# Kernel optimization log

Hardware: AMD Instinct MI355X
Metric: run time of the kernel (lower is better)

The kernel has to match this reference:

```python
import jax, jax.numpy as jnp
import numpy as np


def setup_inputs() -> dict:
    key = jax.random.key(0)
    k1, k2, k3 = jax.random.split(key, 3)
    B, L, D = 8, 4096, 320
    CB_DIM, N_BOOKS = 16, 8192
    input_values = jax.random.normal(k1, (B, L, D), dtype=jnp.float32)
    # mask all ones -> static masked-select shape N = B*L
    mask_time_indices = jnp.ones((B, L), dtype=jnp.int32)
    # xavier_uniform for Linear(D -> CB_DIM, bias=False): limit = sqrt(6/(fan_in+fan_out))
    limit = float(np.sqrt(6.0 / (D + CB_DIM)))
    proj_weight = jax.random.uniform(k2, (CB_DIM, D), dtype=jnp.float32, minval=-limit, maxval=limit)
    code_book = jax.random.normal(k3, (N_BOOKS, CB_DIM), dtype=jnp.float32)
    return {"input_values": input_values, "mask_time_indices": mask_time_indices,
            "proj_weight": proj_weight, "code_book": code_book}


def reference(input_values, mask_time_indices, proj_weight, code_book):
    # input_values: [B, L, D]; mask is all-ones so masked select == flatten (static shape N=B*L)
    B, L, D = input_values.shape
    flat = input_values.reshape(B * L, D)  # [N, D]
    targets = flat @ proj_weight.T  # [N, cb_dim]  (random projection, no bias)
    # argmin over Euclidean norm == argmin over squared distance (monotone),
    # expanded form avoids the [N, n_books, cb_dim] broadcast intermediate.
    t2 = jnp.sum(targets * targets, axis=-1, keepdims=True)        # [N, 1]
    c2 = jnp.sum(code_book * code_book, axis=-1)                   # [n_books]
    d2 = t2 - 2.0 * (targets @ code_book.T) + c2                   # [N, n_books]
    labels = jnp.argmin(d2, axis=-1)                               # [N]
    return labels
```

## Files before the change

### kernel.cpp

```cpp
#include <hip/hip_runtime.h>

#define N_ROWS 32768
#define D_IN 320
#define CB 16
#define N_BOOKS 8192

typedef __attribute__((ext_vector_type(8))) short bf16x8;
typedef __attribute__((ext_vector_type(4))) float f32x4;
#define MFMA __builtin_amdgcn_mfma_f32_16x16x32_bf16
#define AS1 __attribute__((address_space(1)))
#define AS3 __attribute__((address_space(3)))

__device__ __forceinline__ unsigned short bf16rn(float f) {
  unsigned u = __float_as_uint(f);
  u += 0x7fffu + ((u >> 16) & 1u);
  return (unsigned short)(u >> 16);
}
__device__ __forceinline__ float bf16tof(unsigned short h) {
  return __uint_as_float(((unsigned)h) << 16);
}
__device__ __forceinline__ void gload_lds16(const short* g, short* l) {
  __builtin_amdgcn_global_load_lds((const AS1 unsigned int*)g, (AS3 unsigned int*)l, 16, 0, 0);
}

__global__ __launch_bounds__(256, 2) void proj_prep_kernel(
    const float* __restrict__ x, const float* __restrict__ w, short* __restrict__ tsplit,
    const float* __restrict__ cbk, short* __restrict__ bfrag, float* __restrict__ nh_g,
    int* __restrict__ ctr) {
  __shared__ __align__(16) short wfrag[3][10][64][8];
  __shared__ __align__(16) float xs[2][64 * 36];
  const int tid = threadIdx.x;

  if (blockIdx.x >= 512) {
    const int bid = blockIdx.x - 512;
    if (bid == 0 && tid == 0) *ctr = 0;
    const int j = bid * 256 + tid;
    const float4* src = (const float4*)(cbk + (size_t)j * CB);
    float4 a = src[0], b = src[1], c = src[2], d = src[3];
    float ce[16] = {a.x, a.y, a.z, a.w, b.x, b.y, b.z, b.w,
                    c.x, c.y, c.z, c.w, d.x, d.y, d.z, d.w};
    short c1[16], c2[16];
    double s = 0.0;
#pragma unroll
    for (int i = 0; i < 16; i++) {
      s += (double)ce[i] * (double)ce[i];
      unsigned short x1 = bf16rn(ce[i]);
      float r1 = ce[i] - bf16tof(x1);
      unsigned short x2 = bf16rn(r1);
      c1[i] = (short)x1; c2[i] = (short)x2;
    }
    nh_g[j] = (float)(-0.5 * s);
    bf16x8 lo1, hi1, lo2, hi2;
#pragma unroll
    for (int i = 0; i < 8; i++) {
      lo1[i] = c1[i]; hi1[i] = c1[i + 8];
      lo2[i] = c2[i]; hi2[i] = c2[i + 8];
    }
    const int bt = j >> 4, n = j & 15;
    short* base = bfrag + (size_t)bt * 1024;
    *(bf16x8*)(base + (0 * 16 + n) * 8) = lo1;
    *(bf16x8*)(base + (1 * 16 + n) * 8) = hi1;
    *(bf16x8*)(base + (2 * 16 + n) * 8) = lo1;
    *(bf16x8*)(base + (3 * 16 + n) * 8) = hi1;
    *(bf16x8*)(base + 512 + (0 * 16 + n) * 8) = lo2;
    *(bf16x8*)(base + 512 + (1 * 16 + n) * 8) = hi2;
    *(bf16x8*)(base + 512 + (2 * 16 + n) * 8) = lo2;
    *(bf16x8*)(base + 512 + (3 * 16 + n) * 8) = hi2;
    return;
  }

  const int lane = tid & 63;
  const int wv = tid >> 6;

  for (int i = tid; i < D_IN * CB; i += 256) {
    int d = i >> 4, o = i & 15;
    float f = w[o * D_IN + d];
    unsigned short h1 = bf16rn(f);
    float r1 = f - bf16tof(h1);
    unsigned short h2 = bf16rn(r1);
    float r2 = r1 - bf16tof(h2);
    unsigned short h3 = bf16rn(r2);
    int c = d >> 5, qq = (d >> 3) & 3, pos = d & 7;
    int ln = qq * 16 + o;
    wfrag[0][c][ln][pos] = (short)h1;
    wfrag[1][c][ln][pos] = (short)h2;
    wfrag[2][c][ln][pos] = (short)h3;
  }

  const float* xblk = x + (size_t)blockIdx.x * 64 * D_IN;
  {
    int row = tid >> 2, k0 = (tid & 3) * 8;
    float4 v0 = *(const float4*)(xblk + row * D_IN + k0);
    float4 v1 = *(const float4*)(xblk + row * D_IN + k0 + 4);
    *(float4*)&xs[0][row * 36 + k0] = v0;
    *(float4*)&xs[0][row * 36 + k0 + 4] = v1;
  }
  __syncthreads();

  const int m = lane & 15, q = lane >> 4;
  f32x4 g1 = {0.f, 0.f, 0.f, 0.f}, g2 = {0.f, 0.f, 0.f, 0.f}, g3 = {0.f, 0.f, 0.f, 0.f};
  for (int c = 0; c < 10; c++) {
    const int buf = c & 1;
    if (c < 9) {
      int row = tid >> 2, k0 = (tid & 3) * 8;
      float4 v0 = *(const float4*)(xblk + row * D_IN + (c + 1) * 32 + k0);
      float4 v1 = *(const float4*)(xblk + row * D_IN + (c + 1) * 32 + k0 + 4);
      *(float4*)&xs[buf ^ 1][row * 36 + k0] = v0;
      *(float4*)&xs[buf ^ 1][row * 36 + k0 + 4] = v1;
    }
    const float* xp = &xs[buf][(wv * 16 + m) * 36 + q * 8];
    float4 xa = *(const float4*)xp;
    float4 xb = *(const float4*)(xp + 4);
    float xe[8] = {xa.x, xa.y, xa.z, xa.w, xb.x, xb.y, xb.z, xb.w};
    bf16x8 a1, a2, a3;
#pragma unroll
    for (int j = 0; j < 8; j++) {
      unsigned short h1 = bf16rn(xe[j]);
      float r1 = xe[j] - bf16tof(h1);
      unsigned short h2 = bf16rn(r1);
      float r2 = r1 - bf16tof(h2);
      unsigned short h3 = bf16rn(r2);
      a1[j] = (short)h1; a2[j] = (short)h2; a3[j] = (short)h3;
    }
    bf16x8 b1 = *(const bf16x8*)wfrag[0][c][lane];
    bf16x8 b2 = *(const bf16x8*)wfrag[1][c][lane];
    bf16x8 b3 = *(const bf16x8*)wfrag[2][c][lane];
    g1 = MFMA(a1, b1, g1, 0, 0, 0);
    g2 = MFMA(a2, b1, g2, 0, 0, 0);
    g2 = MFMA(a1, b2, g2, 0, 0, 0);
    g3 = MFMA(a3, b1, g3, 0, 0, 0);
    g3 = MFMA(a1, b3, g3, 0, 0, 0);
    g3 = MFMA(a2, b2, g3, 0, 0, 0);
    __syncthreads();
  }

  float* tl = (float*)xs;
#pragma unroll
  for (int r = 0; r < 4; r++) {
    double t = (double)g1[r] + ((double)g2[r] + (double)g3[r]);
    tl[(wv * 16 + q * 4 + r) * 17 + m] = (float)t;
  }
  __syncthreads();
  {
    int row_l = tid >> 2, p = tid & 3;
    short h1[4], h2[4], h3[4];
#pragma unroll
    for (int i = 0; i < 4; i++) {
      float f = tl[row_l * 17 + p * 4 + i];
      unsigned short a = bf16rn(f);
      float r1 = f - bf16tof(a);
      unsigned short b = bf16rn(r1);
      float r2 = r1 - bf16tof(b);
      unsigned short cc = bf16rn(r2);
      h1[i] = (short)a; h2[i] = (short)b; h3[i] = (short)cc;
    }
    size_t base = (size_t)(blockIdx.x * 64 + row_l) * 48;
    *(short4*)(tsplit + base + p * 4) = make_short4(h1[0], h1[1], h1[2], h1[3]);
    *(short4*)(tsplit + base + 16 + p * 4) = make_short4(h2[0], h2[1], h2[2], h2[3]);
    *(short4*)(tsplit + base + 32 + p * 4) = make_short4(h3[0], h3[1], h3[2], h3[3]);
  }
}

#define SC_H 16

__global__ __launch_bounds__(256, 4) void score_kernel(const short* __restrict__ tsplit,
                                                       const short* __restrict__ bfrag,
                                                       const float* __restrict__ nh_g,
                                                       float4* __restrict__ cand) {
  __shared__ __align__(16) short ldsb[2][4096];
  __shared__ float ldsnh[512];
  const int tid = threadIdx.x;
  const int lane = tid & 63;
  const int wv = tid >> 6;
  const int m = lane & 15, q = lane >> 4;
  const int rb = blockIdx.x & 127;
  const int h = blockIdx.x >> 7;
  const int rowbase = rb * 256;

  bf16x8 A12[4];
#pragma unroll
  for (int rt = 0; rt < 4; rt++) {
    int row = rowbase + wv * 64 + rt * 16 + m;
    A12[rt] = *(const bf16x8*)(tsplit + (size_t)row * 48 + q * 8);
  }
  for (int i = tid; i < 512; i += 256) ldsnh[i] = nh_g[h * 512 + i];

  const short* gq = bfrag + (size_t)h * 32768;
  {
    const short* g0 = gq + wv * 512 + lane * 8;
#pragma unroll
    for (int it = 0; it < 2; it++)
      gload_lds16(g0 + it * 2048, &ldsb[0][it * 2048 + wv * 512]);
  }

  float s1[4][4], s2[4][4];
  int i1[4][4];
#pragma unroll
  for (int rt = 0; rt < 4; rt++)
#pragma unroll
    for (int r = 0; r < 4; r++) { s1[rt][r] = -3.4e38f; s2[rt][r] = -3.4e38f; i1[rt][r] = 0; }

  __syncthreads();

  for (int sc = 0; sc < 8; sc++) {
    const int cur = sc & 1;
    if (sc < 7) {
      const short* gs = gq + (sc + 1) * 4096 + wv * 512 + lane * 8;
#pragma unroll
      for (int it = 0; it < 2; it++)
        gload_lds16(gs + it * 2048, &ldsb[cur ^ 1][it * 2048 + wv * 512]);
    }
#pragma unroll
    for (int bt = 0; bt < 4; bt++) {
      const short* bp = &ldsb[cur][bt * 1024];
      bf16x8 b1 = *(const bf16x8*)(bp + lane * 8);
      bf16x8 b2 = *(const bf16x8*)(bp + 512 + lane * 8);
      const int btg = sc * 4 + bt;
      float nh0 = ldsnh[btg * 16 + m];
      f32x4 ci = {nh0, nh0, nh0, nh0};
      const int colv = h * 512 + btg * 16 + m;
#pragma unroll
      for (int rt = 0; rt < 4; rt++) {
        f32x4 acc = MFMA(A12[rt], b1, ci, 0, 0, 0);
        acc = MFMA(A12[rt], b2, acc, 0, 0, 0);
#pragma unroll
        for (int r = 0; r < 4; r++) {
          float v = acc[r];
          float s1o = s1[rt][r];
          s2[rt][r] = __builtin_amdgcn_fmed3f(v, s1o, s2[rt][r]);
          s1[rt][r] = fmaxf(s1o, v);
          i1[rt][r] = (v > s1o) ? colv : i1[rt][r];
        }
      }
    }
    __syncthreads();
  }

#pragma unroll
  for (int rt = 0; rt < 4; rt++)
#pragma unroll
    for (int r = 0; r < 4; r++) {
      float a1v = s1[rt][r], a2v = s2[rt][r];
      int ai = i1[rt][r];
#pragma unroll
      for (int msk = 1; msk <= 8; msk <<= 1) {
        float o1 = __shfl_xor(a1v, msk);
        float o2 = __shfl_xor(a2v, msk);
        int oi = __shfl_xor(ai, msk);
        if (o1 > a1v) {
          a2v = fmaxf(a1v, o2); a1v = o1; ai = oi;
        } else {
          a2v = fmaxf(a2v, o1);
          if (o1 == a1v && oi < ai) ai = oi;
        }
      }
      if (m == 0) {
        int row = rowbase + wv * 64 + rt * 16 + q * 4 + r;
        cand[(size_t)h * N_ROWS + row] = make_float4(a1v, a2v, __int_as_float(ai), 0.f);
      }
    }
}

#define MARGIN_EPS 1.0e-3f

__global__ __launch_bounds__(256) void merge_flag_kernel(const float4* __restrict__ cand,
                                                         int* __restrict__ out,
                                                         int* __restrict__ list,
                                                         int* __restrict__ ctr) {
  const int r = blockIdx.x * 256 + threadIdx.x;
  float S1 = -3.4e38f, S2 = -3.4e38f;
  int I = 0;
#pragma unroll
  for (int h = 0; h < SC_H; h++) {
    float4 v = cand[(size_t)h * N_ROWS + r];
    if (v.x > S1) {
      S2 = fmaxf(S1, v.y); S1 = v.x; I = __float_as_int(v.z);
    } else {
      S2 = fmaxf(S2, v.x);
    }
  }
  out[r] = I;
  if (S1 - S2 < MARGIN_EPS) {
    int slot = atomicAdd(ctr, 1);
    list[slot] = r;
  }
}

__global__ __launch_bounds__(256) void rescore_kernel(const int* __restrict__ list,
                                                      const int* __restrict__ ctr,
                                                      const float* __restrict__ x,
                                                      const float* __restrict__ w,
                                                      const float* __restrict__ codebook,
                                                      int* __restrict__ out) {
  __shared__ double ps[16][17];
  __shared__ double tsh[16];
  __shared__ double rs[256];
  __shared__ int ri[256];
  const int tid = threadIdx.x;
  const int total = ctr[0];

  for (int it = blockIdx.x; it < total; it += gridDim.x) {
    const int row = list[it];
    {
      int o = tid & 15, c = tid >> 4;
      double p = 0.0;
      for (int k = 0; k < 20; k++) {
        int d = c * 20 + k;
        p = fma((double)x[(size_t)row * D_IN + d], (double)w[o * D_IN + d], p);
      }
      ps[c][o] = p;
    }
    __syncthreads();
    if (tid < 16) {
      double t = 0.0;
      for (int c = 0; c < 16; c++) t += ps[c][tid];
      tsh[tid] = t;
    }
    __syncthreads();
    double t[16];
#pragma unroll
    for (int i = 0; i < 16; i++) t[i] = tsh[i];
    double bs = -1.0e300;
    int bi = 0;
    for (int j = tid; j < N_BOOKS; j += 256) {
      const float* cp = codebook + (size_t)j * CB;
      double dot = 0.0, cc = 0.0;
#pragma unroll
      for (int i = 0; i < 16; i++) {
        double cv = (double)cp[i];
        dot = fma(t[i], cv, dot);
        cc = fma(cv, cv, cc);
      }
      double mv = dot - 0.5 * cc;
      if (mv > bs) { bs = mv; bi = j; }
    }
    rs[tid] = bs; ri[tid] = bi;
    __syncthreads();
    for (int s = 128; s > 0; s >>= 1) {
      if (tid < s) {
        double os = rs[tid + s]; int oi = ri[tid + s];
        if (os > rs[tid] || (os == rs[tid] && oi < ri[tid])) { rs[tid] = os; ri[tid] = oi; }
      }
      __syncthreads();
    }
    if (tid == 0) out[row] = ri[0];
    __syncthreads();
  }
}

extern "C" void kernel_launch(void* const* d_in, const int* in_sizes, int n_in,
                              void* d_out, int out_size, void* d_ws, size_t ws_size,
                              hipStream_t stream) {
  (void)in_sizes; (void)n_in; (void)out_size; (void)ws_size;
  const float* x = (const float*)d_in[0];
  const float* w = (const float*)d_in[2];
  const float* codebook = (const float*)d_in[3];

  char* ws = (char*)d_ws;
  short* tsplit = (short*)(ws);
  short* bfrag = (short*)(ws + (3 << 20));
  float* nh_g = (float*)(ws + (4 << 20));
  int* list = (int*)(ws + 4231168);
  int* ctr = (int*)(ws + 4362240);
  float4* cand = (float4*)(ws + (5 << 20));
  int* out = (int*)d_out;

  proj_prep_kernel<<<512 + N_BOOKS / 256, 256, 0, stream>>>(x, w, tsplit, codebook, bfrag,
                                                            nh_g, ctr);
  score_kernel<<<128 * SC_H, 256, 0, stream>>>(tsplit, bfrag, nh_g, cand);
  merge_flag_kernel<<<N_ROWS / 256, 256, 0, stream>>>(cand, out, list, ctr);
  rescore_kernel<<<512, 256, 0, stream>>>(list, ctr, x, w, codebook, out);
}
```

Before: 190.2 us.

## Use per-wave private codebook buffers with waitcnt instead of block barriers

Each wave now streams its own copy of each 16-code codebook tile into a private double-buffered LDS region. It waits on vmcnt instead of calling __syncthreads, so waves no longer stall on one another. The codebook split drops from 16 to 8 slices, giving each block 1024 codes and halving the candidates to merge; launch bounds relax to 2 blocks per CU. In exchange, every wave fetches the same codebook data redundantly, and there are fewer, longer-running blocks.

After: 188.8 us. Within noise of the previous version (-0.7%).

```diff
diff --git a/kernel.cpp b/kernel.cpp
--- a/kernel.cpp
+++ b/kernel.cpp
@@ -161,14 +161,14 @@
   }
 }
 
-#define SC_H 16
-
-__global__ __launch_bounds__(256, 4) void score_kernel(const short* __restrict__ tsplit,
+#define SC_H 8
+
+__global__ __launch_bounds__(256, 2) void score_kernel(const short* __restrict__ tsplit,
                                                        const short* __restrict__ bfrag,
                                                        const float* __restrict__ nh_g,
                                                        float4* __restrict__ cand) {
-  __shared__ __align__(16) short ldsb[2][4096];
-  __shared__ float ldsnh[512];
+  __shared__ __align__(16) short ldsb[4][2][1024];
+  __shared__ float ldsnh[1024];
   const int tid = threadIdx.x;
   const int lane = tid & 63;
   const int wv = tid >> 6;
@@ -183,15 +183,13 @@
     int row = rowbase + wv * 64 + rt * 16 + m;
     A12[rt] = *(const bf16x8*)(tsplit + (size_t)row * 48 + q * 8);
   }
-  for (int i = tid; i < 512; i += 256) ldsnh[i] = nh_g[h * 512 + i];
-
-  const short* gq = bfrag + (size_t)h * 32768;
-  {
-    const short* g0 = gq + wv * 512 + lane * 8;
-#pragma unroll
-    for (int it = 0; it < 2; it++)
-      gload_lds16(g0 + it * 2048, &ldsb[0][it * 2048 + wv * 512]);
-  }
+  for (int i = tid; i < 1024; i += 256) ldsnh[i] = nh_g[h * 1024 + i];
+
+  const short* gq = bfrag + (size_t)h * 65536 + lane * 8;
+  short* bcur = &ldsb[wv][0][0];
+  short* bnxt = &ldsb[wv][1][0];
+  gload_lds16(gq, bcur);
+  gload_lds16(gq + 512, bcur + 512);
 
   float s1[4][4], s2[4][4];
   int i1[4][4];
@@ -202,38 +200,34 @@
 
   __syncthreads();
 
-  for (int sc = 0; sc < 8; sc++) {
-    const int cur = sc & 1;
-    if (sc < 7) {
-      const short* gs = gq + (sc + 1) * 4096 + wv * 512 + lane * 8;
-#pragma unroll
-      for (int it = 0; it < 2; it++)
-        gload_lds16(gs + it * 2048, &ldsb[cur ^ 1][it * 2048 + wv * 512]);
-    }
-#pragma unroll
-    for (int bt = 0; bt < 4; bt++) {
-      const short* bp = &ldsb[cur][bt * 1024];
-      bf16x8 b1 = *(const bf16x8*)(bp + lane * 8);
-      bf16x8 b2 = *(const bf16x8*)(bp + 512 + lane * 8);
-      const int btg = sc * 4 + bt;
-      float nh0 = ldsnh[btg * 16 + m];
-      f32x4 ci = {nh0, nh0, nh0, nh0};
-      const int colv = h * 512 + btg * 16 + m;
-#pragma unroll
-      for (int rt = 0; rt < 4; rt++) {
-        f32x4 acc = MFMA(A12[rt], b1, ci, 0, 0, 0);
-        acc = MFMA(A12[rt], b2, acc, 0, 0, 0);
-#pragma unroll
-        for (int r = 0; r < 4; r++) {
-          float v = acc[r];
-          float s1o = s1[rt][r];
-          s2[rt][r] = __builtin_amdgcn_fmed3f(v, s1o, s2[rt][r]);
-          s1[rt][r] = fmaxf(s1o, v);
-          i1[rt][r] = (v > s1o) ? colv : i1[rt][r];
-        }
-      }
-    }
-    __syncthreads();
+  for (int bt = 0; bt < 64; bt++) {
+    if (bt < 63) {
+      const short* gs = gq + (bt + 1) * 1024;
+      gload_lds16(gs, bnxt);
+      gload_lds16(gs + 512, bnxt + 512);
+      asm volatile("s_waitcnt vmcnt(2)" ::: "memory");
+    } else {
+      asm volatile("s_waitcnt vmcnt(0)" ::: "memory");
+    }
+    bf16x8 b1 = *(const bf16x8*)(bcur + lane * 8);
+    bf16x8 b2 = *(const bf16x8*)(bcur + 512 + lane * 8);
+    float nh0 = ldsnh[bt * 16 + m];
+    f32x4 ci = {nh0, nh0, nh0, nh0};
+    const int colv = h * 1024 + bt * 16 + m;
+#pragma unroll
+    for (int rt = 0; rt < 4; rt++) {
+      f32x4 acc = MFMA(A12[rt], b1, ci, 0, 0, 0);
+      acc = MFMA(A12[rt], b2, acc, 0, 0, 0);
+#pragma unroll
+      for (int r = 0; r < 4; r++) {
+        float v = acc[r];
+        float s1o = s1[rt][r];
+        s2[rt][r] = __builtin_amdgcn_fmed3f(v, s1o, s2[rt][r]);
+        s1[rt][r] = fmaxf(s1o, v);
+        i1[rt][r] = (v > s1o) ? colv : i1[rt][r];
+      }
+    }
+    short* t = bcur; bcur = bnxt; bnxt = t;
   }
 
 #pragma unroll
```

## Pack column tag into score mantissa and halve codebook column splits

Applied to the files above, without the earlier changes.

The running top-2 no longer tracks an argmax index per accumulator. Instead, a 6-bit tile tag is packed into the low mantissa bits of each score, so the inner loop is just mask/or, med3 and max. The winning lane inside each 16-lane group is recovered once at the end with a ballot. Each block now covers 1024 codebook columns instead of 512 (SC_H 16→8), with doubled LDS buffers and launch bounds lowered to 2 blocks per SIMD. This trades a slight loss of score precision (absorbed by the existing margin recheck) and lower occupancy for fewer VALU ops per MFMA output and less candidate traffic to the merge kernel.

Measured after the change: 179.4 us. 5.7% less time.

```diff
diff --git a/kernel.cpp b/kernel.cpp
--- a/kernel.cpp
+++ b/kernel.cpp
@@ -161,14 +161,14 @@
   }
 }
 
-#define SC_H 16
-
-__global__ __launch_bounds__(256, 4) void score_kernel(const short* __restrict__ tsplit,
+#define SC_H 8
+
+__global__ __launch_bounds__(256, 2) void score_kernel(const short* __restrict__ tsplit,
                                                        const short* __restrict__ bfrag,
                                                        const float* __restrict__ nh_g,
                                                        float4* __restrict__ cand) {
-  __shared__ __align__(16) short ldsb[2][4096];
-  __shared__ float ldsnh[512];
+  __shared__ __align__(16) short ldsb[2][8192];
+  __shared__ float ldsnh[1024];
   const int tid = threadIdx.x;
   const int lane = tid & 63;
   const int wv = tid >> 6;
@@ -183,53 +183,51 @@
     int row = rowbase + wv * 64 + rt * 16 + m;
     A12[rt] = *(const bf16x8*)(tsplit + (size_t)row * 48 + q * 8);
   }
-  for (int i = tid; i < 512; i += 256) ldsnh[i] = nh_g[h * 512 + i];
-
-  const short* gq = bfrag + (size_t)h * 32768;
+  for (int i = tid; i < 1024; i += 256) ldsnh[i] = nh_g[h * 1024 + i];
+
+  const short* gq = bfrag + (size_t)h * 65536;
   {
     const short* g0 = gq + wv * 512 + lane * 8;
 #pragma unroll
-    for (int it = 0; it < 2; it++)
+    for (int it = 0; it < 4; it++)
       gload_lds16(g0 + it * 2048, &ldsb[0][it * 2048 + wv * 512]);
   }
 
+  const unsigned qmask = 0xFFFFFFC0u;
   float s1[4][4], s2[4][4];
-  int i1[4][4];
 #pragma unroll
   for (int rt = 0; rt < 4; rt++)
 #pragma unroll
-    for (int r = 0; r < 4; r++) { s1[rt][r] = -3.4e38f; s2[rt][r] = -3.4e38f; i1[rt][r] = 0; }
+    for (int r = 0; r < 4; r++) { s1[rt][r] = -3.4e38f; s2[rt][r] = -3.4e38f; }
 
   __syncthreads();
 
   for (int sc = 0; sc < 8; sc++) {
     const int cur = sc & 1;
     if (sc < 7) {
-      const short* gs = gq + (sc + 1) * 4096 + wv * 512 + lane * 8;
-#pragma unroll
-      for (int it = 0; it < 2; it++)
+      const short* gs = gq + (sc + 1) * 8192 + wv * 512 + lane * 8;
+#pragma unroll
+      for (int it = 0; it < 4; it++)
         gload_lds16(gs + it * 2048, &ldsb[cur ^ 1][it * 2048 + wv * 512]);
     }
 #pragma unroll
-    for (int bt = 0; bt < 4; bt++) {
+    for (int bt = 0; bt < 8; bt++) {
       const short* bp = &ldsb[cur][bt * 1024];
       bf16x8 b1 = *(const bf16x8*)(bp + lane * 8);
       bf16x8 b2 = *(const bf16x8*)(bp + 512 + lane * 8);
-      const int btg = sc * 4 + bt;
+      const int btg = sc * 8 + bt;
       float nh0 = ldsnh[btg * 16 + m];
       f32x4 ci = {nh0, nh0, nh0, nh0};
-      const int colv = h * 512 + btg * 16 + m;
+      const unsigned tagv = (unsigned)(63 - btg);
 #pragma unroll
       for (int rt = 0; rt < 4; rt++) {
         f32x4 acc = MFMA(A12[rt], b1, ci, 0, 0, 0);
         acc = MFMA(A12[rt], b2, acc, 0, 0, 0);
 #pragma unroll
         for (int r = 0; r < 4; r++) {
-          float v = acc[r];
-          float s1o = s1[rt][r];
-          s2[rt][r] = __builtin_amdgcn_fmed3f(v, s1o, s2[rt][r]);
-          s1[rt][r] = fmaxf(s1o, v);
-          i1[rt][r] = (v > s1o) ? colv : i1[rt][r];
+          float vq = __uint_as_float((__float_as_uint(acc[r]) & qmask) | tagv);
+          s2[rt][r] = __builtin_amdgcn_fmed3f(vq, s1[rt][r], s2[rt][r]);
+          s1[rt][r] = fmaxf(s1[rt][r], vq);
         }
       }
     }
@@ -240,23 +238,23 @@
   for (int rt = 0; rt < 4; rt++)
 #pragma unroll
     for (int r = 0; r < 4; r++) {
-      float a1v = s1[rt][r], a2v = s2[rt][r];
-      int ai = i1[rt][r];
+      float s1v = s1[rt][r], s2v = s2[rt][r];
+      const float ps1 = s1v;
 #pragma unroll
       for (int msk = 1; msk <= 8; msk <<= 1) {
-        float o1 = __shfl_xor(a1v, msk);
-        float o2 = __shfl_xor(a2v, msk);
-        int oi = __shfl_xor(ai, msk);
-        if (o1 > a1v) {
-          a2v = fmaxf(a1v, o2); a1v = o1; ai = oi;
-        } else {
-          a2v = fmaxf(a2v, o1);
-          if (o1 == a1v && oi < ai) ai = oi;
-        }
-      }
+        float o1 = __shfl_xor(s1v, msk);
+        float o2 = __shfl_xor(s2v, msk);
+        s2v = __builtin_amdgcn_fmed3f(s1v, o1, fmaxf(s2v, o2));
+        s1v = fmaxf(s1v, o1);
+      }
+      unsigned long long bal = __ballot(ps1 == s1v);
+      unsigned grp = (unsigned)((bal >> (q * 16)) & 0xFFFFull);
+      int mwin = __builtin_ctz(grp | 0x10000u);
+      int btwin = 63 - (int)(__float_as_uint(s1v) & 63u);
+      int col = h * 1024 + btwin * 16 + mwin;
       if (m == 0) {
         int row = rowbase + wv * 64 + rt * 16 + q * 4 + r;
-        cand[(size_t)h * N_ROWS + row] = make_float4(a1v, a2v, __int_as_float(ai), 0.f);
+        cand[(size_t)h * N_ROWS + row] = make_float4(s1v, s2v, __int_as_float(col), 0.f);
       }
     }
 }
```
